# Kernel tuning notes

Hardware: AMD Instinct MI355X
Metric: run time of the kernel (lower is better)

Reference implementation:

```python
import jax, jax.numpy as jnp
import numpy as np

N = 256   # input_size
H = 512   # hidden_size
B = 128   # batch


def _make_masks(n, h):
    # Replicates MADE.create_masks with n_hidden=1
    d_in = np.arange(n)
    d_h = np.arange(h) % (n - 1)
    d_out = np.arange(n) % n - 1  # = arange(n) - 1
    m0 = (d_h[:, None] >= d_in[None, :]).astype(np.float32)   # (H, N)
    m1 = (d_h[:, None] >= d_h[None, :]).astype(np.float32)    # (H, H)
    m2 = (d_out[:, None] >= d_h[None, :]).astype(np.float32)  # (N, H)
    m2 = np.tile(m2, (2, 1))                                   # (2N, H)
    return jnp.asarray(m0), jnp.asarray(m1), jnp.asarray(m2)


def setup_inputs() -> dict:
    key = jax.random.key(0)
    ks = jax.random.split(key, 7)
    s = 0.02
    return {
        "z": jax.random.normal(ks[0], (B, N), jnp.float32),
        "w0": jax.random.normal(ks[1], (H, N), jnp.float32) * s,
        "b0": jax.random.normal(ks[2], (H,), jnp.float32) * s,
        "w1": jax.random.normal(ks[3], (H, H), jnp.float32) * s,
        "b1": jax.random.normal(ks[4], (H,), jnp.float32) * s,
        "w2": jax.random.normal(ks[5], (2 * N, H), jnp.float32) * s,
        "b2": jax.random.normal(ks[6], (2 * N,), jnp.float32) * s,
    }


def reference(z, w0, b0, w1, b1, w2, b2):
    m0, m1, m2 = _make_masks(N, H)
    mw0 = m0 * w0
    mw1 = m1 * w1
    mw2 = m2 * w2

    def net(x):
        h = jax.nn.relu(x @ mw0.T + b0)
        h = jax.nn.relu(h @ mw1.T + b1)
        return h @ mw2.T + b2  # (B, 2N)

    def step(carry, i):
        x, log_det = carry
        out = net(x)
        mu = out[:, i]          # (B,)
        alpha = out[:, N + i]   # (B,)
        x = x.at[:, i].set(mu + z[:, i] * jnp.exp(alpha))
        return (x, log_det + alpha), None

    x0 = jnp.zeros_like(z)
    ld0 = jnp.zeros((z.shape[0],), z.dtype)
    (x, log_det), _ = jax.lax.scan(step, (x0, ld0), jnp.arange(N))
    return x, -log_det
```

## Files before the change

kernel.cpp:

```cpp
#include <hip/hip_runtime.h>

#define NN 256
#define HH 512
#define BB 128
#define PKS (5 * HH)

__global__ __launch_bounds__(512)
void made_prep(const float* __restrict__ w0,
               const float* __restrict__ w1,
               const float* __restrict__ w2,
               float* __restrict__ pk) {
    const int i = blockIdx.x;
    const int k = threadIdx.x;
    const int lev = k % 255;
    float* row = pk + (size_t)i * PKS;
    row[k]          = (lev < i)  ? w2[i * HH + k]        : 0.f;
    row[HH + k]     = (lev < i)  ? w2[(NN + i) * HH + k] : 0.f;
    row[2*HH + k]   = (lev >= i) ? w0[k * NN + i]        : 0.f;
    const int l1 = i % 255;
    row[3*HH + k]   = (lev >= l1) ? w1[k * HH + i]       : 0.f;
    const int j2 = i + 255;
    const int l2 = j2 % 255;
    row[4*HH + k]   = (lev >= l2) ? w1[k * HH + j2]      : 0.f;
}

struct B10 { float4 q0,q1,q2,q3,q4,q5,q6,q7,q8,q9; };

__device__ __forceinline__ float4 ld4(const float* p) { return *(const float4*)p; }

__device__ __forceinline__ void load_all(B10& b, const float* p, int o8) {
    b.q0 = ld4(p + o8);          b.q1 = ld4(p + o8 + 4);
    b.q2 = ld4(p + HH + o8);     b.q3 = ld4(p + HH + o8 + 4);
    b.q4 = ld4(p + 2*HH + o8);   b.q5 = ld4(p + 2*HH + o8 + 4);
    b.q6 = ld4(p + 3*HH + o8);   b.q7 = ld4(p + 3*HH + o8 + 4);
    b.q8 = ld4(p + 4*HH + o8);   b.q9 = ld4(p + 4*HH + o8 + 4);
}

__device__ __forceinline__ float rl_f(float v, int lane) {
    return __int_as_float(__builtin_amdgcn_readlane(__float_as_int(v), lane));
}

__device__ __forceinline__ float q45c(const B10& b, int s) {
    switch (s) {
        case 0: return b.q4.x; case 1: return b.q4.y;
        case 2: return b.q4.z; case 3: return b.q4.w;
        case 4: return b.q5.x; case 5: return b.q5.y;
        case 6: return b.q5.z; default: return b.q5.w;
    }
}

#define DPP_ADD(v, ctrl, rm) \
    ((v) + __int_as_float(__builtin_amdgcn_update_dpp(0, __float_as_int(v), (ctrl), (rm), 0xf, false)))

__device__ __forceinline__ void reduce2(float& pm, float& pa) {
    pm = DPP_ADD(pm, 0x111, 0xf);  pa = DPP_ADD(pa, 0x111, 0xf);
    pm = DPP_ADD(pm, 0x112, 0xf);  pa = DPP_ADD(pa, 0x112, 0xf);
    pm = DPP_ADD(pm, 0x114, 0xf);  pa = DPP_ADD(pa, 0x114, 0xf);
    pm = DPP_ADD(pm, 0x118, 0xf);  pa = DPP_ADD(pa, 0x118, 0xf);
    pm = DPP_ADD(pm, 0x142, 0xa);  pa = DPP_ADD(pa, 0x142, 0xa);
    pm = DPP_ADD(pm, 0x143, 0xc);  pa = DPP_ADD(pa, 0x143, 0xc);
}

#define DOT8(res, A, B)  do {                                   \
    float t01_ = fmaf(h_[1], (A).y, h_[0] * (A).x);             \
    float t23_ = fmaf(h_[3], (A).w, h_[2] * (A).z);             \
    float t45_ = fmaf(h_[5], (B).y, h_[4] * (B).x);             \
    float t67_ = fmaf(h_[7], (B).w, h_[6] * (B).z);             \
    res = (t01_ + t23_) + (t45_ + t67_);                        \
} while (0)

#define STEP(g, r, BUF) do {                                                 \
    const int i_  = ((g) << 3) | (r);                                        \
    const float* pf_ = pk + (size_t)((i_ + 2) & 255) * PKS;                  \
    float h_[8];                                                             \
    h_[0] = fmaxf(a1v[0], 0.f); h_[1] = fmaxf(a1v[1], 0.f);                  \
    h_[2] = fmaxf(a1v[2], 0.f); h_[3] = fmaxf(a1v[3], 0.f);                  \
    h_[4] = fmaxf(a1v[4], 0.f); h_[5] = fmaxf(a1v[5], 0.f);                  \
    h_[6] = fmaxf(a1v[6], 0.f); h_[7] = fmaxf(a1v[7], 0.f);                  \
    float pm_, pa_;                                                          \
    DOT8(pm_, BUF.q0, BUF.q1);                                               \
    DOT8(pa_, BUF.q2, BUF.q3);                                               \
    BUF.q0 = ld4(pf_ + o8);        BUF.q1 = ld4(pf_ + o8 + 4);               \
    BUF.q2 = ld4(pf_ + HH + o8);   BUF.q3 = ld4(pf_ + HH + o8 + 4);          \
    reduce2(pm_, pa_);                                                       \
    const int sB_ = ((r) + 7) & 7;                                           \
    const int LB_ = ((r) == 0) ? ((g) + 31) : ((g) + 32);                    \
    const int zl_ = ((g) << 1) + ((r) >> 2);                                 \
    float a0A_ = rl_f(a0v[(r)], (g));                                        \
    float w0A_ = rl_f(q45c(BUF, (r)), (g));                                  \
    float a0B_ = rl_f(a0v[sB_], LB_);                                        \
    float w0B_ = rl_f(q45c(BUF, sB_), LB_);                                  \
    float tm_ = rl_f(pm_, 63), ta_ = rl_f(pa_, 63);                          \
    float mu_ = tm_ + rl_f(b2v[(r)], (g));                                   \
    float al_ = ta_ + rl_f(b2v[(r)], (g) + 32);                              \
    ldacc += al_;                                                            \
    float zi_ = rl_f(zrv[(r) & 3], zl_);                                     \
    float xi_ = fmaf(zi_, __expf(al_), mu_);                                 \
    xo[(r) & 3] = (t == zl_) ? xi_ : xo[(r) & 3];                            \
    float h0a_ = fmaxf(fmaf(xi_, w0A_, a0A_), 0.f);                          \
    float h0b_ = fmaxf(fmaf(xi_, w0B_, a0B_), 0.f);                          \
    if ((r) < 2 && (g) == 0) {          \
        float a0C_ = rl_f(a0v[6 + (r)], 63);                                 \
        float w0C_ = rl_f(q45c(BUF, 6 + (r)), 63);                           \
        float h0c_ = fmaxf(fmaf(xi_, w0C_, a0C_), 0.f);                      \
        const float* wc_ = ((r) == 0) ? w1c0v : w1c1v;                       \
        a1v[0] = fmaf(h0c_, wc_[0], a1v[0]); a1v[1] = fmaf(h0c_, wc_[1], a1v[1]); \
        a1v[2] = fmaf(h0c_, wc_[2], a1v[2]); a1v[3] = fmaf(h0c_, wc_[3], a1v[3]); \
        a1v[4] = fmaf(h0c_, wc_[4], a1v[4]); a1v[5] = fmaf(h0c_, wc_[5], a1v[5]); \
        a1v[6] = fmaf(h0c_, wc_[6], a1v[6]); a1v[7] = fmaf(h0c_, wc_[7], a1v[7]); \
    }                                                                        \
    a0v[0] = fmaf(xi_, BUF.q4.x, a0v[0]); a0v[1] = fmaf(xi_, BUF.q4.y, a0v[1]); \
    a0v[2] = fmaf(xi_, BUF.q4.z, a0v[2]); a0v[3] = fmaf(xi_, BUF.q4.w, a0v[3]); \
    a0v[4] = fmaf(xi_, BUF.q5.x, a0v[4]); a0v[5] = fmaf(xi_, BUF.q5.y, a0v[5]); \
    a0v[6] = fmaf(xi_, BUF.q5.z, a0v[6]); a0v[7] = fmaf(xi_, BUF.q5.w, a0v[7]); \
    BUF.q4 = ld4(pf_ + 2*HH + o8); BUF.q5 = ld4(pf_ + 2*HH + o8 + 4);        \
    a1v[0] = fmaf(h0b_, BUF.q8.x, fmaf(h0a_, BUF.q6.x, a1v[0]));             \
    a1v[1] = fmaf(h0b_, BUF.q8.y, fmaf(h0a_, BUF.q6.y, a1v[1]));             \
    a1v[2] = fmaf(h0b_, BUF.q8.z, fmaf(h0a_, BUF.q6.z, a1v[2]));             \
    a1v[3] = fmaf(h0b_, BUF.q8.w, fmaf(h0a_, BUF.q6.w, a1v[3]));             \
    a1v[4] = fmaf(h0b_, BUF.q9.x, fmaf(h0a_, BUF.q7.x, a1v[4]));             \
    a1v[5] = fmaf(h0b_, BUF.q9.y, fmaf(h0a_, BUF.q7.y, a1v[5]));             \
    a1v[6] = fmaf(h0b_, BUF.q9.z, fmaf(h0a_, BUF.q7.z, a1v[6]));             \
    a1v[7] = fmaf(h0b_, BUF.q9.w, fmaf(h0a_, BUF.q7.w, a1v[7]));             \
    BUF.q6 = ld4(pf_ + 3*HH + o8); BUF.q7 = ld4(pf_ + 3*HH + o8 + 4);        \
    BUF.q8 = ld4(pf_ + 4*HH + o8); BUF.q9 = ld4(pf_ + 4*HH + o8 + 4);        \
} while (0)

__global__ __launch_bounds__(64, 1)
void made_seq64(const float* __restrict__ z,
                const float* __restrict__ b0g,
                const float* __restrict__ b1g,
                const float* __restrict__ b2g,
                const float* __restrict__ w1,
                const float* __restrict__ pk,
                float* __restrict__ out) {
    const int bb = blockIdx.x;
    const int t  = threadIdx.x;
    const int o8 = t << 3;

    float a0v[8], a1v[8], b2v[8];
    {
        float4 a = ld4(b0g + o8), b = ld4(b0g + o8 + 4);
        a0v[0]=a.x; a0v[1]=a.y; a0v[2]=a.z; a0v[3]=a.w;
        a0v[4]=b.x; a0v[5]=b.y; a0v[6]=b.z; a0v[7]=b.w;
        a = ld4(b1g + o8); b = ld4(b1g + o8 + 4);
        a1v[0]=a.x; a1v[1]=a.y; a1v[2]=a.z; a1v[3]=a.w;
        a1v[4]=b.x; a1v[5]=b.y; a1v[6]=b.z; a1v[7]=b.w;
        a = ld4(b2g + o8); b = ld4(b2g + o8 + 4);
        b2v[0]=a.x; b2v[1]=a.y; b2v[2]=a.z; b2v[3]=a.w;
        b2v[4]=b.x; b2v[5]=b.y; b2v[6]=b.z; b2v[7]=b.w;
    }
    float w1c0v[8], w1c1v[8];
    #pragma unroll
    for (int j = 0; j < 8; ++j) {
        const int k = o8 + j;
        w1c0v[j] = w1[k * HH + 510];
        w1c1v[j] = ((k % 255) >= 1) ? w1[k * HH + 511] : 0.f;
    }
    float4 z4 = ld4(z + (bb << 8) + (t << 2));
    float zrv[4] = {z4.x, z4.y, z4.z, z4.w};
    float xo[4]  = {0.f, 0.f, 0.f, 0.f};
    float ldacc  = 0.f;

    B10 Ba, Bb;
    load_all(Ba, pk, o8);
    load_all(Bb, pk + PKS, o8);

    for (int g = 0; g < 32; ++g) {
        STEP(g, 0, Ba); STEP(g, 1, Bb); STEP(g, 2, Ba); STEP(g, 3, Bb);
        STEP(g, 4, Ba); STEP(g, 5, Bb); STEP(g, 6, Ba); STEP(g, 7, Bb);
    }

    *(float4*)(out + (bb << 8) + (t << 2)) = make_float4(xo[0], xo[1], xo[2], xo[3]);
    if (t == 0) out[BB * NN + bb] = -ldacc;
}

__global__ __launch_bounds__(256)
void made_seq_fb(const float* __restrict__ z,
                 const float* __restrict__ w0, const float* __restrict__ b0,
                 const float* __restrict__ w1, const float* __restrict__ b1,
                 const float* __restrict__ w2, const float* __restrict__ b2,
                 float* __restrict__ out) {
    const int bb = blockIdx.x;
    const int t  = threadIdx.x;
    const int u0 = t, u1 = t + 256;
    const int l0 = u0 % 255, s0 = u0 / 255;
    const int l1 = u1 % 255, s1 = u1 / 255;
    const int wave = t >> 6, lane = t & 63;

    __shared__ float red[2][4][2];
    __shared__ float pub[2][3][2];

    float a0_0 = b0[u0], a0_1 = b0[u1];
    float a1_0 = b1[u0], a1_1 = b1[u1];
    float ld = 0.f;

    for (int i = 0; i < NN; ++i) {
        float cw2m0 = (l0 < i) ? w2[i * HH + u0] : 0.f;
        float cw2a0 = (l0 < i) ? w2[(NN + i) * HH + u0] : 0.f;
        float cw2m1 = (l1 < i) ? w2[i * HH + u1] : 0.f;
        float cw2a1 = (l1 < i) ? w2[(NN + i) * HH + u1] : 0.f;
        float cw00  = (l0 >= i) ? w0[u0 * NN + i] : 0.f;
        float cw01  = (l1 >= i) ? w0[u1 * NN + i] : 0.f;
        bool g0 = (l0 >= (i % 255)), g1 = (l1 >= (i % 255));
        float w1a0 = g0 ? w1[u0 * HH + i] : 0.f;
        float w1a1 = g1 ? w1[u1 * HH + i] : 0.f;
        float w1b0 = g0 ? w1[u0 * HH + i + 255] : 0.f;
        float w1b1 = g1 ? w1[u1 * HH + i + 255] : 0.f;

        float h10 = fmaxf(a1_0, 0.f), h11 = fmaxf(a1_1, 0.f);
        float pm = h10 * cw2m0 + h11 * cw2m1;
        float pa = h10 * cw2a0 + h11 * cw2a1;
        #pragma unroll
        for (int offs = 32; offs > 0; offs >>= 1) {
            pm += __shfl_xor(pm, offs);
            pa += __shfl_xor(pa, offs);
        }
        const int bf = i & 1;
        if (lane == 0) { red[bf][wave][0] = pm; red[bf][wave][1] = pa; }
        if (l0 == i) { pub[bf][s0][0] = a0_0; pub[bf][s0][1] = cw00; }
        if (l1 == i) { pub[bf][s1][0] = a0_1; pub[bf][s1][1] = cw01; }
        __syncthreads();

        float mu = b2[i]      + red[bf][0][0] + red[bf][1][0] + red[bf][2][0] + red[bf][3][0];
        float al = b2[NN + i] + red[bf][0][1] + red[bf][1][1] + red[bf][2][1] + red[bf][3][1];
        ld += al;
        float xi = fmaf(z[bb * NN + i], __expf(al), mu);
        if (t == 0) out[bb * NN + i] = xi;

        a0_0 = fmaf(xi, cw00, a0_0);
        a0_1 = fmaf(xi, cw01, a0_1);

        float h0a = fmaxf(fmaf(xi, pub[bf][0][1], pub[bf][0][0]), 0.f);
        float h0b = fmaxf(fmaf(xi, pub[bf][1][1], pub[bf][1][0]), 0.f);
        a1_0 = fmaf(h0a, w1a0, a1_0);
        a1_1 = fmaf(h0a, w1a1, a1_1);
        a1_0 = fmaf(h0b, w1b0, a1_0);
        a1_1 = fmaf(h0b, w1b1, a1_1);
        if (i < 2) {
            float w1c0 = (l0 >= i) ? w1[u0 * HH + i + 510] : 0.f;
            float w1c1 = (l1 >= i) ? w1[u1 * HH + i + 510] : 0.f;
            float h0c = fmaxf(fmaf(xi, pub[bf][2][1], pub[bf][2][0]), 0.f);
            a1_0 = fmaf(h0c, w1c0, a1_0);
            a1_1 = fmaf(h0c, w1c1, a1_1);
        }
        __syncthreads();
    }

    if (t == 0) out[BB * NN + bb] = -ld;
}

extern "C" void kernel_launch(void* const* d_in, const int* in_sizes, int n_in,
                              void* d_out, int out_size, void* d_ws, size_t ws_size,
                              hipStream_t stream) {
    const float* z  = (const float*)d_in[0];
    const float* w0 = (const float*)d_in[1];
    const float* b0 = (const float*)d_in[2];
    const float* w1 = (const float*)d_in[3];
    const float* b1 = (const float*)d_in[4];
    const float* w2 = (const float*)d_in[5];
    const float* b2 = (const float*)d_in[6];
    float* out = (float*)d_out;

    const size_t need = (size_t)NN * PKS * sizeof(float);
    if (ws_size >= need) {
        float* pk = (float*)d_ws;
        made_prep<<<NN, 512, 0, stream>>>(w0, w1, w2, pk);
        made_seq64<<<BB, 64, 0, stream>>>(z, b0, b1, b2, w1, pk, out);
    } else {
        made_seq_fb<<<BB, 256, 0, stream>>>(z, w0, b0, w1, b1, w2, b2, out);
    }
}
```

Before: 92.44 us.

## Stream per-step weight slices into LDS via async global_load_lds ring buffer

The sequential 64-thread kernel used to prefetch each step's packed weight row from global memory into a double-buffered set of registers. It now issues asynchronous global-to-LDS loads three steps ahead into a 4-slot LDS ring and reads each slice back with ten ds_read_b128 instructions. The per-thread layout also changes from 8 contiguous hidden units to two strided groups of 4, which changes the readlane indexing. The aim is to hide global latency further ahead and free registers. In exchange it adds a full vmcnt(0) and lgkmcnt(0) wait every step, which may serialize the pipeline.

```diff
diff --git a/kernel.cpp b/kernel.cpp
--- a/kernel.cpp
+++ b/kernel.cpp
@@ -4,6 +4,11 @@
 #define HH 512
 #define BB 128
 #define PKS (5 * HH)
+
+typedef float f32x4 __attribute__((ext_vector_type(4)));
+typedef __attribute__((address_space(3))) float       lds_f;
+typedef __attribute__((address_space(3))) void        lds_v;
+typedef __attribute__((address_space(1))) const void  glb_v;
 
 __global__ __launch_bounds__(512)
 void made_prep(const float* __restrict__ w0,
@@ -24,29 +29,14 @@
     row[4*HH + k]   = (lev >= l2) ? w1[k * HH + j2]      : 0.f;
 }
 
-struct B10 { float4 q0,q1,q2,q3,q4,q5,q6,q7,q8,q9; };
-
-__device__ __forceinline__ float4 ld4(const float* p) { return *(const float4*)p; }
-
-__device__ __forceinline__ void load_all(B10& b, const float* p, int o8) {
-    b.q0 = ld4(p + o8);          b.q1 = ld4(p + o8 + 4);
-    b.q2 = ld4(p + HH + o8);     b.q3 = ld4(p + HH + o8 + 4);
-    b.q4 = ld4(p + 2*HH + o8);   b.q5 = ld4(p + 2*HH + o8 + 4);
-    b.q6 = ld4(p + 3*HH + o8);   b.q7 = ld4(p + 3*HH + o8 + 4);
-    b.q8 = ld4(p + 4*HH + o8);   b.q9 = ld4(p + 4*HH + o8 + 4);
-}
-
 __device__ __forceinline__ float rl_f(float v, int lane) {
     return __int_as_float(__builtin_amdgcn_readlane(__float_as_int(v), lane));
 }
 
-__device__ __forceinline__ float q45c(const B10& b, int s) {
-    switch (s) {
-        case 0: return b.q4.x; case 1: return b.q4.y;
-        case 2: return b.q4.z; case 3: return b.q4.w;
-        case 4: return b.q5.x; case 5: return b.q5.y;
-        case 6: return b.q5.z; default: return b.q5.w;
-    }
+__device__ __forceinline__ f32x4 ld4(const float* p) { return *(const f32x4*)p; }
+
+__device__ __forceinline__ void gld16(const float* g, float* l) {
+    __builtin_amdgcn_global_load_lds((glb_v*)g, (lds_v*)l, 16, 0, 0);
 }
 
 #define DPP_ADD(v, ctrl, rm) \
@@ -61,69 +51,103 @@
     pm = DPP_ADD(pm, 0x143, 0xc);  pa = DPP_ADD(pa, 0x143, 0xc);
 }
 
-#define DOT8(res, A, B)  do {                                   \
-    float t01_ = fmaf(h_[1], (A).y, h_[0] * (A).x);             \
-    float t23_ = fmaf(h_[3], (A).w, h_[2] * (A).z);             \
-    float t45_ = fmaf(h_[5], (B).y, h_[4] * (B).x);             \
-    float t67_ = fmaf(h_[7], (B).w, h_[6] * (B).z);             \
-    res = (t01_ + t23_) + (t45_ + t67_);                        \
-} while (0)
-
-#define STEP(g, r, BUF) do {                                                 \
-    const int i_  = ((g) << 3) | (r);                                        \
-    const float* pf_ = pk + (size_t)((i_ + 2) & 255) * PKS;                  \
-    float h_[8];                                                             \
-    h_[0] = fmaxf(a1v[0], 0.f); h_[1] = fmaxf(a1v[1], 0.f);                  \
-    h_[2] = fmaxf(a1v[2], 0.f); h_[3] = fmaxf(a1v[3], 0.f);                  \
-    h_[4] = fmaxf(a1v[4], 0.f); h_[5] = fmaxf(a1v[5], 0.f);                  \
-    h_[6] = fmaxf(a1v[6], 0.f); h_[7] = fmaxf(a1v[7], 0.f);                  \
-    float pm_, pa_;                                                          \
-    DOT8(pm_, BUF.q0, BUF.q1);                                               \
-    DOT8(pa_, BUF.q2, BUF.q3);                                               \
-    BUF.q0 = ld4(pf_ + o8);        BUF.q1 = ld4(pf_ + o8 + 4);               \
-    BUF.q2 = ld4(pf_ + HH + o8);   BUF.q3 = ld4(pf_ + HH + o8 + 4);          \
+#define LDS_READ10(VA)                                                       \
+    asm volatile(                                                            \
+        "ds_read_b128 %0, %10 offset:0\n\t"                                  \
+        "ds_read_b128 %1, %10 offset:1024\n\t"                               \
+        "ds_read_b128 %2, %10 offset:2048\n\t"                               \
+        "ds_read_b128 %3, %10 offset:3072\n\t"                               \
+        "ds_read_b128 %4, %10 offset:4096\n\t"                               \
+        "ds_read_b128 %5, %10 offset:5120\n\t"                               \
+        "ds_read_b128 %6, %10 offset:6144\n\t"                               \
+        "ds_read_b128 %7, %10 offset:7168\n\t"                               \
+        "ds_read_b128 %8, %10 offset:8192\n\t"                               \
+        "ds_read_b128 %9, %10 offset:9216"                                   \
+        : "=&v"(qA0), "=&v"(qA1), "=&v"(qB0), "=&v"(qB1), "=&v"(qC0),        \
+          "=&v"(qC1), "=&v"(qD0), "=&v"(qD1), "=&v"(qE0), "=&v"(qE1)         \
+        : "v"(VA))
+
+#define STEP(g, r) do {                                                      \
+    const int i_ = ((g) << 3) | (r);                                         \
+    asm volatile("s_waitcnt vmcnt(0)" ::: "memory");    \
+    __builtin_amdgcn_sched_barrier(0);                                       \
+    f32x4 qA0, qA1, qB0, qB1, qC0, qC1, qD0, qD1, qE0, qE1;                  \
+    const unsigned va_ = ((r)&3)==0 ? va0 : ((r)&3)==1 ? va1                 \
+                       : ((r)&3)==2 ? va2 : va3;                             \
+    LDS_READ10(va_);                                                         \
+    asm volatile("s_waitcnt lgkmcnt(0)" ::: "memory");                       \
+    __builtin_amdgcn_sched_barrier(0);                                       \
+         \
+    {                                                                        \
+        const float* gs_ = pk + (size_t)((i_ + 3) & 255) * PKS + 4 * t;      \
+        float* ls_ = lds4 + (((r) + 3) & 3) * 2560;                          \
+        gld16(gs_,        ls_       ); gld16(gs_ + 256,  ls_ + 256 );        \
+        gld16(gs_ + 512,  ls_ + 512 ); gld16(gs_ + 768,  ls_ + 768 );        \
+        gld16(gs_ + 1024, ls_ + 1024); gld16(gs_ + 1280, ls_ + 1280);        \
+        gld16(gs_ + 1536, ls_ + 1536); gld16(gs_ + 1792, ls_ + 1792);        \
+        gld16(gs_ + 2048, ls_ + 2048); gld16(gs_ + 2304, ls_ + 2304);        \
+    }                                                                        \
+    __builtin_amdgcn_sched_barrier(0);                                       \
+                                            \
+    float h0_=fmaxf(a1lo[0],0.f), h1_=fmaxf(a1lo[1],0.f);                    \
+    float h2_=fmaxf(a1lo[2],0.f), h3_=fmaxf(a1lo[3],0.f);                    \
+    float h4_=fmaxf(a1hi[0],0.f), h5_=fmaxf(a1hi[1],0.f);                    \
+    float h6_=fmaxf(a1hi[2],0.f), h7_=fmaxf(a1hi[3],0.f);                    \
+    float pm_ = (fmaf(h1_,qA0[1],h0_*qA0[0]) + fmaf(h3_,qA0[3],h2_*qA0[2]))  \
+              + (fmaf(h5_,qA1[1],h4_*qA1[0]) + fmaf(h7_,qA1[3],h6_*qA1[2])); \
+    float pa_ = (fmaf(h1_,qB0[1],h0_*qB0[0]) + fmaf(h3_,qB0[3],h2_*qB0[2]))  \
+              + (fmaf(h5_,qB1[1],h4_*qB1[0]) + fmaf(h7_,qB1[3],h6_*qB1[2])); \
     reduce2(pm_, pa_);                                                       \
-    const int sB_ = ((r) + 7) & 7;                                           \
-    const int LB_ = ((r) == 0) ? ((g) + 31) : ((g) + 32);                    \
-    const int zl_ = ((g) << 1) + ((r) >> 2);                                 \
-    float a0A_ = rl_f(a0v[(r)], (g));                                        \
-    float w0A_ = rl_f(q45c(BUF, (r)), (g));                                  \
-    float a0B_ = rl_f(a0v[sB_], LB_);                                        \
-    float w0B_ = rl_f(q45c(BUF, sB_), LB_);                                  \
+    const int Li_ = 2*(g) + ((r)>>2);                                        \
     float tm_ = rl_f(pm_, 63), ta_ = rl_f(pa_, 63);                          \
-    float mu_ = tm_ + rl_f(b2v[(r)], (g));                                   \
-    float al_ = ta_ + rl_f(b2v[(r)], (g) + 32);                              \
+    float mu_ = tm_ + rl_f(b2lo[(r)&3], Li_);                                \
+    float al_ = ta_ + rl_f(b2hi[(r)&3], Li_);                                \
     ldacc += al_;                                                            \
-    float zi_ = rl_f(zrv[(r) & 3], zl_);                                     \
+    float zi_ = rl_f(zrv[(r)&3], Li_);                                       \
     float xi_ = fmaf(zi_, __expf(al_), mu_);                                 \
-    xo[(r) & 3] = (t == zl_) ? xi_ : xo[(r) & 3];                            \
+    xo[(r)&3] = (t == Li_) ? xi_ : xo[(r)&3];                                \
+                        \
+    float a0A_ = rl_f(a0lo[(r)&3], Li_);                                     \
+    float w0A_ = rl_f(qC0[(r)&3], Li_);                                      \
+    float a0B_, w0B_;                                                        \
+    if ((r) == 0) {     \
+        const int lbn_ = 2*(g) - 1;                                          \
+        float aB0_ = rl_f(a0lo[3], 63), wB0_ = rl_f(qC0[3], 63);             \
+        float aBn_ = rl_f(a0hi[3], lbn_), wBn_ = rl_f(qC1[3], lbn_);         \
+        a0B_ = ((g) == 0) ? aB0_ : aBn_;                                     \
+        w0B_ = ((g) == 0) ? wB0_ : wBn_;                                     \
+    } else {                                    \
+        const int lb_ = 2*(g) + (((r)-1)>>2);                                \
+        a0B_ = rl_f(a0hi[((r)-1)&3], lb_);                                   \
+        w0B_ = rl_f(qC1[((r)-1)&3], lb_);                                    \
+    }                                                                        \
     float h0a_ = fmaxf(fmaf(xi_, w0A_, a0A_), 0.f);                          \
     float h0b_ = fmaxf(fmaf(xi_, w0B_, a0B_), 0.f);                          \
-    if ((r) < 2 && (g) == 0) {          \
-        float a0C_ = rl_f(a0v[6 + (r)], 63);                                 \
-        float w0C_ = rl_f(q45c(BUF, 6 + (r)), 63);                           \
-        float h0c_ = fmaxf(fmaf(xi_, w0C_, a0C_), 0.f);                      \
-        const float* wc_ = ((r) == 0) ? w1c0v : w1c1v;                       \
-        a1v[0] = fmaf(h0c_, wc_[0], a1v[0]); a1v[1] = fmaf(h0c_, wc_[1], a1v[1]); \
-        a1v[2] = fmaf(h0c_, wc_[2], a1v[2]); a1v[3] = fmaf(h0c_, wc_[3], a1v[3]); \
-        a1v[4] = fmaf(h0c_, wc_[4], a1v[4]); a1v[5] = fmaf(h0c_, wc_[5], a1v[5]); \
-        a1v[6] = fmaf(h0c_, wc_[6], a1v[6]); a1v[7] = fmaf(h0c_, wc_[7], a1v[7]); \
+    if ((r) < 2) {        \
+        if ((g) == 0) {                                                      \
+            float a0C_ = ((r)==0) ? rl_f(a0hi[2],63) : rl_f(a0hi[3],63);     \
+            float w0C_ = ((r)==0) ? rl_f(qC1[2],63) : rl_f(qC1[3],63);       \
+            float h0c_ = fmaxf(fmaf(xi_, w0C_, a0C_), 0.f);                  \
+            f32x4 wl_ = ((r)==0) ? w1cAlo : w1cBlo;                          \
+            f32x4 wh_ = ((r)==0) ? w1cAhi : w1cBhi;                          \
+            a1lo[0]=fmaf(h0c_,wl_[0],a1lo[0]); a1lo[1]=fmaf(h0c_,wl_[1],a1lo[1]); \
+            a1lo[2]=fmaf(h0c_,wl_[2],a1lo[2]); a1lo[3]=fmaf(h0c_,wl_[3],a1lo[3]); \
+            a1hi[0]=fmaf(h0c_,wh_[0],a1hi[0]); a1hi[1]=fmaf(h0c_,wh_[1],a1hi[1]); \
+            a1hi[2]=fmaf(h0c_,wh_[2],a1hi[2]); a1hi[3]=fmaf(h0c_,wh_[3],a1hi[3]); \
+        }                                                                    \
     }                                                                        \
-    a0v[0] = fmaf(xi_, BUF.q4.x, a0v[0]); a0v[1] = fmaf(xi_, BUF.q4.y, a0v[1]); \
-    a0v[2] = fmaf(xi_, BUF.q4.z, a0v[2]); a0v[3] = fmaf(xi_, BUF.q4.w, a0v[3]); \
-    a0v[4] = fmaf(xi_, BUF.q5.x, a0v[4]); a0v[5] = fmaf(xi_, BUF.q5.y, a0v[5]); \
-    a0v[6] = fmaf(xi_, BUF.q5.z, a0v[6]); a0v[7] = fmaf(xi_, BUF.q5.w, a0v[7]); \
-    BUF.q4 = ld4(pf_ + 2*HH + o8); BUF.q5 = ld4(pf_ + 2*HH + o8 + 4);        \
-    a1v[0] = fmaf(h0b_, BUF.q8.x, fmaf(h0a_, BUF.q6.x, a1v[0]));             \
-    a1v[1] = fmaf(h0b_, BUF.q8.y, fmaf(h0a_, BUF.q6.y, a1v[1]));             \
-    a1v[2] = fmaf(h0b_, BUF.q8.z, fmaf(h0a_, BUF.q6.z, a1v[2]));             \
-    a1v[3] = fmaf(h0b_, BUF.q8.w, fmaf(h0a_, BUF.q6.w, a1v[3]));             \
-    a1v[4] = fmaf(h0b_, BUF.q9.x, fmaf(h0a_, BUF.q7.x, a1v[4]));             \
-    a1v[5] = fmaf(h0b_, BUF.q9.y, fmaf(h0a_, BUF.q7.y, a1v[5]));             \
-    a1v[6] = fmaf(h0b_, BUF.q9.z, fmaf(h0a_, BUF.q7.z, a1v[6]));             \
-    a1v[7] = fmaf(h0b_, BUF.q9.w, fmaf(h0a_, BUF.q7.w, a1v[7]));             \
-    BUF.q6 = ld4(pf_ + 3*HH + o8); BUF.q7 = ld4(pf_ + 3*HH + o8 + 4);        \
-    BUF.q8 = ld4(pf_ + 4*HH + o8); BUF.q9 = ld4(pf_ + 4*HH + o8 + 4);        \
+    a0lo[0]=fmaf(xi_,qC0[0],a0lo[0]); a0lo[1]=fmaf(xi_,qC0[1],a0lo[1]);      \
+    a0lo[2]=fmaf(xi_,qC0[2],a0lo[2]); a0lo[3]=fmaf(xi_,qC0[3],a0lo[3]);      \
+    a0hi[0]=fmaf(xi_,qC1[0],a0hi[0]); a0hi[1]=fmaf(xi_,qC1[1],a0hi[1]);      \
+    a0hi[2]=fmaf(xi_,qC1[2],a0hi[2]); a0hi[3]=fmaf(xi_,qC1[3],a0hi[3]);      \
+    a1lo[0]=fmaf(h0b_,qE0[0],fmaf(h0a_,qD0[0],a1lo[0]));                     \
+    a1lo[1]=fmaf(h0b_,qE0[1],fmaf(h0a_,qD0[1],a1lo[1]));                     \
+    a1lo[2]=fmaf(h0b_,qE0[2],fmaf(h0a_,qD0[2],a1lo[2]));                     \
+    a1lo[3]=fmaf(h0b_,qE0[3],fmaf(h0a_,qD0[3],a1lo[3]));                     \
+    a1hi[0]=fmaf(h0b_,qE1[0],fmaf(h0a_,qD1[0],a1hi[0]));                     \
+    a1hi[1]=fmaf(h0b_,qE1[1],fmaf(h0a_,qD1[1],a1hi[1]));                     \
+    a1hi[2]=fmaf(h0b_,qE1[2],fmaf(h0a_,qD1[2],a1hi[2]));                     \
+    a1hi[3]=fmaf(h0b_,qE1[3],fmaf(h0a_,qD1[3],a1hi[3]));                     \
 } while (0)
 
 __global__ __launch_bounds__(64, 1)
@@ -134,44 +158,48 @@
                 const float* __restrict__ w1,
                 const float* __restrict__ pk,
                 float* __restrict__ out) {
+    __shared__ float lds4[4 * 2560];
     const int bb = blockIdx.x;
     const int t  = threadIdx.x;
-    const int o8 = t << 3;
-
-    float a0v[8], a1v[8], b2v[8];
-    {
-        float4 a = ld4(b0g + o8), b = ld4(b0g + o8 + 4);
-        a0v[0]=a.x; a0v[1]=a.y; a0v[2]=a.z; a0v[3]=a.w;
-        a0v[4]=b.x; a0v[5]=b.y; a0v[6]=b.z; a0v[7]=b.w;
-        a = ld4(b1g + o8); b = ld4(b1g + o8 + 4);
-        a1v[0]=a.x; a1v[1]=a.y; a1v[2]=a.z; a1v[3]=a.w;
-        a1v[4]=b.x; a1v[5]=b.y; a1v[6]=b.z; a1v[7]=b.w;
-        a = ld4(b2g + o8); b = ld4(b2g + o8 + 4);
-        b2v[0]=a.x; b2v[1]=a.y; b2v[2]=a.z; b2v[3]=a.w;
-        b2v[4]=b.x; b2v[5]=b.y; b2v[6]=b.z; b2v[7]=b.w;
-    }
-    float w1c0v[8], w1c1v[8];
+
+    f32x4 a0lo = ld4(b0g + 4*t), a0hi = ld4(b0g + 256 + 4*t);
+    f32x4 a1lo = ld4(b1g + 4*t), a1hi = ld4(b1g + 256 + 4*t);
+    f32x4 b2lo = ld4(b2g + 4*t), b2hi = ld4(b2g + 256 + 4*t);
+    f32x4 zrv  = ld4(z + (bb << 8) + 4*t);
+    f32x4 xo   = {0.f, 0.f, 0.f, 0.f};
+    f32x4 w1cAlo, w1cAhi, w1cBlo, w1cBhi;
     #pragma unroll
-    for (int j = 0; j < 8; ++j) {
-        const int k = o8 + j;
-        w1c0v[j] = w1[k * HH + 510];
-        w1c1v[j] = ((k % 255) >= 1) ? w1[k * HH + 511] : 0.f;
-    }
-    float4 z4 = ld4(z + (bb << 8) + (t << 2));
-    float zrv[4] = {z4.x, z4.y, z4.z, z4.w};
-    float xo[4]  = {0.f, 0.f, 0.f, 0.f};
-    float ldacc  = 0.f;
-
-    B10 Ba, Bb;
-    load_all(Ba, pk, o8);
-    load_all(Bb, pk + PKS, o8);
+    for (int c = 0; c < 4; ++c) {
+        const int kl = 4*t + c, kh = 256 + 4*t + c;
+        w1cAlo[c] = w1[kl * HH + 510];
+        w1cAhi[c] = w1[kh * HH + 510];
+        w1cBlo[c] = ((kl % 255) >= 1) ? w1[kl * HH + 511] : 0.f;
+        w1cBhi[c] = ((kh % 255) >= 1) ? w1[kh * HH + 511] : 0.f;
+    }
+    float ldacc = 0.f;
+
+    const unsigned lbase = (unsigned)(unsigned long long)(lds_f*)&lds4[0];
+    const unsigned va0 = lbase + 16u * (unsigned)t;
+    const unsigned va1 = va0 + 10240u, va2 = va0 + 20480u, va3 = va0 + 30720u;
+
+    __builtin_amdgcn_sched_barrier(0);
+    #pragma unroll
+    for (int s = 0; s < 3; ++s) {
+        const float* gs = pk + (size_t)s * PKS + 4*t;
+        float* ls = lds4 + s * 2560;
+        #pragma unroll
+        for (int j = 0; j < 10; ++j) gld16(gs + 256*j, ls + 256*j);
+    }
+    __builtin_amdgcn_sched_barrier(0);
 
     for (int g = 0; g < 32; ++g) {
-        STEP(g, 0, Ba); STEP(g, 1, Bb); STEP(g, 2, Ba); STEP(g, 3, Bb);
-        STEP(g, 4, Ba); STEP(g, 5, Bb); STEP(g, 6, Ba); STEP(g, 7, Bb);
-    }
-
-    *(float4*)(out + (bb << 8) + (t << 2)) = make_float4(xo[0], xo[1], xo[2], xo[3]);
+        STEP(g, 0); STEP(g, 1); STEP(g, 2); STEP(g, 3);
+        STEP(g, 4); STEP(g, 5); STEP(g, 6); STEP(g, 7);
+    }
+
+    asm volatile("s_waitcnt vmcnt(0)" ::: "memory");
+    __builtin_amdgcn_sched_barrier(0);
+    *(f32x4*)(out + (bb << 8) + 4*t) = xo;
     if (t == 0) out[BB * NN + bb] = -ldacc;
 }
 
```

Result: slower. 166.6 us (+80.2%).
